# Optimization experiments

Measured on AMD Instinct MI355X. Metric: run time of the kernel, lower is better.

Reference implementation:

```python
import jax, jax.numpy as jnp
import numpy as np

T, B, D = 256, 256, 512
H, DK = 8, 64          # num_heads, d_kv; inner_dim = H*DK = 512
NUM_GROUPS = 16


def setup_inputs() -> dict:
    key = jax.random.key(0)
    ks = jax.random.split(key, 6)
    hidden_states = jax.random.normal(ks[0], (T, B, D), dtype=jnp.float32)
    # sorted group ids over the batch axis (what _infer_group_ids_from_mask recovers)
    group_ids = jnp.sort(jax.random.randint(ks[1], (B,), 0, NUM_GROUPS, dtype=jnp.int32))
    scale = 1.0 / np.sqrt(D)
    Wq = jax.random.normal(ks[2], (D, H * DK), dtype=jnp.float32) * scale
    Wk = jax.random.normal(ks[3], (D, H * DK), dtype=jnp.float32) * scale
    Wv = jax.random.normal(ks[4], (D, H * DK), dtype=jnp.float32) * scale
    Wo = jax.random.normal(ks[5], (H * DK, D), dtype=jnp.float32) * scale
    return {"hidden_states": hidden_states, "group_ids": group_ids,
            "Wq": Wq, "Wk": Wk, "Wv": Wv, "Wo": Wo}


def reference(hidden_states, group_ids, Wq, Wk, Wv, Wo):
    # Group-restricted self-attention along the batch axis, per time step & head.
    # Equivalent to the block-sparse MiniFlash kernel: entries attend only to
    # batch entries with the same group id.
    t, b, d = hidden_states.shape
    q = (hidden_states @ Wq).reshape(t, b, H, DK)
    k = (hidden_states @ Wk).reshape(t, b, H, DK)
    v = (hidden_states @ Wv).reshape(t, b, H, DK)
    sm_scale = 1.0 / np.sqrt(DK)
    # scores: [T, H, B, B] over the batch axis
    scores = jnp.einsum("tihd,tjhd->thij", q, k) * sm_scale
    allowed = group_ids[:, None] == group_ids[None, :]          # [B, B]
    neg = jnp.finfo(scores.dtype).min
    scores = jnp.where(allowed[None, None, :, :], scores, neg)
    attn = jax.nn.softmax(scores, axis=-1)
    out = jnp.einsum("thij,tjhd->tihd", attn, v).reshape(t, b, H * DK)
    return out @ Wo
```

## Files before the change

kernel.cpp:

```cpp
#include <hip/hip_runtime.h>
#include <hip/hip_bf16.h>

typedef __attribute__((ext_vector_type(8))) short short8;
typedef __attribute__((ext_vector_type(4))) short short4v;
typedef __attribute__((ext_vector_type(4))) float f32x4;

#define MFMA16(a, b, c) __builtin_amdgcn_mfma_f32_16x16x32_bf16(a, b, c, 0, 0, 0)

__device__ __forceinline__ unsigned short f2bf(float f) {
    union { __hip_bfloat16 h; unsigned short u; } v;
    v.h = __float2bfloat16(f);
    return v.u;
}

__device__ __forceinline__ short8 pack8(float4 a, float4 b) {
    short8 p;
    p[0] = (short)f2bf(a.x); p[1] = (short)f2bf(a.y);
    p[2] = (short)f2bf(a.z); p[3] = (short)f2bf(a.w);
    p[4] = (short)f2bf(b.x); p[5] = (short)f2bf(b.y);
    p[6] = (short)f2bf(b.z); p[7] = (short)f2bf(b.w);
    return p;
}

__device__ __forceinline__ int swz64(int row, int bytecol) {
    return row * 64 + ((bytecol ^ ((row & 7) << 4)) >> 1);
}
__device__ __forceinline__ int swz256(int row, int bytecol) {
    return row * 256 + ((bytecol ^ ((row & 7) << 4)) >> 1);
}

__global__ __launch_bounds__(256) void wprep(
    const float* __restrict__ Wq, const float* __restrict__ Wk,
    const float* __restrict__ Wv, const float* __restrict__ Wo,
    unsigned short* __restrict__ wt)
{
    __shared__ float tile[64][65];
    const int bid = blockIdx.x;
    const int m = bid >> 6, tb = bid & 63;
    const int kr = (tb >> 3) << 6, nc = (tb & 7) << 6;
    const float* W = (m == 0) ? Wq : (m == 1) ? Wk : (m == 2) ? Wv : Wo;
    const int tid = threadIdx.x;
    for (int i = tid; i < 4096; i += 256)
        tile[i >> 6][i & 63] = W[(size_t)(kr + (i >> 6)) * 512 + nc + (i & 63)];
    __syncthreads();
    unsigned short* dst = wt + (size_t)m * 262144;
    for (int i = tid; i < 4096; i += 256)
        dst[(size_t)(nc + (i >> 6)) * 512 + kr + (i & 63)] = f2bf(tile[i & 63][i >> 6]);
}

__global__ __launch_bounds__(1024, 4) void qkv_attn_mfma(
    const float* __restrict__ hs,
    const int*   __restrict__ gid,
    const float* __restrict__ Wq, const float* __restrict__ Wk,
    const float* __restrict__ Wv,
    const unsigned short* __restrict__ wt,
    float*       __restrict__ out)
{
    __shared__ unsigned short Xs[256 * 64];
    __shared__ unsigned short Wsh[192 * 64];
    __shared__ unsigned short Ksh[256 * 64];
    __shared__ unsigned short Vt[64 * 256];
    __shared__ unsigned short XP[256 * 64];
    __shared__ int sgid[256];
    __shared__ int glo[16], ghi[16];

    const int bid = blockIdx.x;
    const int h   = (bid & 63) >> 3;
    const int t   = ((bid >> 6) << 3) + (bid & 7);

    const int tid  = threadIdx.x;
    const int lane = tid & 63;
    const int w    = tid >> 6;
    const int l15  = lane & 15;
    const int hi4  = lane >> 4;
    const int mg   = w & 3;
    const int ng   = w >> 2;

    if (tid < 16) { glo[tid] = 256; ghi[tid] = -1; }
    __syncthreads();
    if (tid < 256) {
        const int g = gid[tid];
        sgid[tid] = g;
        atomicMin(&glo[g], tid);
        atomicMax(&ghi[g], tid);
    }

    const float* __restrict__ Xbase = hs + (size_t)t * (256 * 512);

    const int xr = tid >> 2, xq = tid & 3;
    const bool doW = tid < 768;
    const int wc = tid >> 2;
    const int wq = tid & 3;
    const int wmat = wc >> 6, wcol = wc & 63;
    const unsigned short* __restrict__ wsrc =
        wt ? wt + ((size_t)wmat * 512 + h * 64 + wcol) * 512 : nullptr;
    const float* __restrict__ wfsrc =
        (wmat == 0) ? Wq : (wmat == 1) ? Wk : Wv;

    f32x4 acc[4][3];
    #pragma unroll
    for (int mt = 0; mt < 4; ++mt)
        #pragma unroll
        for (int nt = 0; nt < 3; ++nt)
            acc[mt][nt] = (f32x4){0.f, 0.f, 0.f, 0.f};

    float4 xf[4];
    short8 w8[2];
    {
        const float* s = Xbase + (size_t)xr * 512 + xq * 16;
        xf[0] = *(const float4*)(s + 0);  xf[1] = *(const float4*)(s + 4);
        xf[2] = *(const float4*)(s + 8);  xf[3] = *(const float4*)(s + 12);
        if (doW) {
            if (wt) {
                w8[0] = *(const short8*)(wsrc + wq * 16);
                w8[1] = *(const short8*)(wsrc + wq * 16 + 8);
            } else {
                #pragma unroll
                for (int b = 0; b < 2; ++b)
                    #pragma unroll
                    for (int j = 0; j < 8; ++j)
                        w8[b][j] = (short)f2bf(
                            wfsrc[(size_t)(wq * 16 + b * 8 + j) * 512 + h * 64 + wcol]);
            }
        }
    }

    for (int kb = 0; kb < 512; kb += 64) {
        *(short8*)&Xs[swz64(xr, xq * 32 + 0)]  = pack8(xf[0], xf[1]);
        *(short8*)&Xs[swz64(xr, xq * 32 + 16)] = pack8(xf[2], xf[3]);
        if (doW) {
            *(short8*)&Wsh[swz64(wc, wq * 32 + 0)]  = w8[0];
            *(short8*)&Wsh[swz64(wc, wq * 32 + 16)] = w8[1];
        }
        __syncthreads();
        if (kb < 448) {
            const int kn = kb + 64;
            const float* s = Xbase + (size_t)xr * 512 + kn + xq * 16;
            xf[0] = *(const float4*)(s + 0);  xf[1] = *(const float4*)(s + 4);
            xf[2] = *(const float4*)(s + 8);  xf[3] = *(const float4*)(s + 12);
            if (doW) {
                if (wt) {
                    w8[0] = *(const short8*)(wsrc + kn + wq * 16);
                    w8[1] = *(const short8*)(wsrc + kn + wq * 16 + 8);
                } else {
                    #pragma unroll
                    for (int b = 0; b < 2; ++b)
                        #pragma unroll
                        for (int j = 0; j < 8; ++j)
                            w8[b][j] = (short)f2bf(
                                wfsrc[(size_t)(kn + wq * 16 + b * 8 + j) * 512 + h * 64 + wcol]);
                }
            }
        }
        #pragma unroll
        for (int ks = 0; ks < 2; ++ks) {
            short8 af[4];
            #pragma unroll
            for (int mt = 0; mt < 4; ++mt)
                af[mt] = *(const short8*)&Xs[swz64(mg * 64 + mt * 16 + l15,
                                                   ks * 64 + hi4 * 16)];
            __builtin_amdgcn_s_setprio(1);
            #pragma unroll
            for (int nt = 0; nt < 3; ++nt) {
                const short8 bf = *(const short8*)&Wsh[swz64(ng * 48 + nt * 16 + l15,
                                                             ks * 64 + hi4 * 16)];
                #pragma unroll
                for (int mt = 0; mt < 4; ++mt)
                    acc[mt][nt] = MFMA16(af[mt], bf, acc[mt][nt]);
            }
            __builtin_amdgcn_s_setprio(0);
        }
        __syncthreads();
    }

    #pragma unroll
    for (int nt = 0; nt < 3; ++nt) {
        const int c0 = (ng * 3 + nt) * 16;
        const int m  = c0 >> 6;
        const int d0 = c0 & 63;
        #pragma unroll
        for (int mt = 0; mt < 4; ++mt) {
            const int rowb = mg * 64 + mt * 16 + hi4 * 4;
            if (m == 0) {
                #pragma unroll
                for (int r = 0; r < 4; ++r)
                    XP[swz64(rowb + r, (d0 + l15) * 2)] = f2bf(acc[mt][nt][r]);
            } else if (m == 1) {
                #pragma unroll
                for (int r = 0; r < 4; ++r)
                    Ksh[swz64(rowb + r, (d0 + l15) * 2)] = f2bf(acc[mt][nt][r]);
            } else {
                short4v vv;
                #pragma unroll
                for (int r = 0; r < 4; ++r) vv[r] = (short)f2bf(acc[mt][nt][r]);
                *(short4v*)&Vt[swz256(d0 + l15, rowb * 2)] = vv;
            }
        }
    }
    __syncthreads();

    const int wrow = w << 4;
    int rg[4];
    #pragma unroll
    for (int r = 0; r < 4; ++r) rg[r] = sgid[wrow + hi4 * 4 + r];
    const int klo = glo[sgid[wrow]];
    const int khi = ghi[sgid[wrow + 15]];

    short8 qf[2];
    #pragma unroll
    for (int ks = 0; ks < 2; ++ks)
        qf[ks] = *(const short8*)&XP[swz64(wrow + l15, ks * 64 + hi4 * 16)];

    f32x4 o[4];
    float mrun[4], lrun[4];
    #pragma unroll
    for (int n = 0; n < 4; ++n) o[n] = (f32x4){0.f, 0.f, 0.f, 0.f};
    #pragma unroll
    for (int r = 0; r < 4; ++r) { mrun[r] = -3.0e38f; lrun[r] = 0.f; }

    for (int kc = klo & ~63; kc <= khi; kc += 64) {
        f32x4 sfr[4];
        __builtin_amdgcn_s_setprio(1);
        #pragma unroll
        for (int n = 0; n < 4; ++n) {
            const int krow = kc + n * 16 + l15;
            const short8 kf0 = *(const short8*)&Ksh[swz64(krow, hi4 * 16)];
            const short8 kf1 = *(const short8*)&Ksh[swz64(krow, 64 + hi4 * 16)];
            f32x4 z = (f32x4){0.f, 0.f, 0.f, 0.f};
            z = MFMA16(qf[0], kf0, z);
            z = MFMA16(qf[1], kf1, z);
            sfr[n] = z;
        }
        __builtin_amdgcn_s_setprio(0);
        int cg[4];
        #pragma unroll
        for (int n = 0; n < 4; ++n) cg[n] = sgid[kc + n * 16 + l15];

        #pragma unroll
        for (int r = 0; r < 4; ++r) {
            const int gr = rg[r];
            float sv[4];
            float smax = -3.0e38f;
            #pragma unroll
            for (int n = 0; n < 4; ++n) {
                float x = sfr[n][r] * 0.125f;
                x = (cg[n] == gr) ? x : -3.0e38f;
                sv[n] = x;
                smax = fmaxf(smax, x);
            }
            smax = fmaxf(smax, __shfl_xor(smax, 1));
            smax = fmaxf(smax, __shfl_xor(smax, 2));
            smax = fmaxf(smax, __shfl_xor(smax, 4));
            smax = fmaxf(smax, __shfl_xor(smax, 8));
            const float newm = fmaxf(mrun[r], smax);
            const float corr = __expf(mrun[r] - newm);
            float ps = 0.f;
            unsigned short pb[4];
            #pragma unroll
            for (int n = 0; n < 4; ++n) {
                const float p = (sv[n] > -1.0e38f) ? __expf(sv[n] - newm) : 0.f;
                ps += p;
                pb[n] = f2bf(p);
            }
            ps += __shfl_xor(ps, 1); ps += __shfl_xor(ps, 2);
            ps += __shfl_xor(ps, 4); ps += __shfl_xor(ps, 8);
            lrun[r] = lrun[r] * corr + ps;
            mrun[r] = newm;
            #pragma unroll
            for (int n = 0; n < 4; ++n) o[n][r] *= corr;
            const int prow = wrow + hi4 * 4 + r;
            #pragma unroll
            for (int n = 0; n < 4; ++n)
                XP[swz64(prow, (n * 16 + l15) * 2)] = pb[n];
        }

        const short8 pa0 = *(const short8*)&XP[swz64(wrow + l15, hi4 * 16)];
        const short8 pa1 = *(const short8*)&XP[swz64(wrow + l15, 64 + hi4 * 16)];
        __builtin_amdgcn_s_setprio(1);
        #pragma unroll
        for (int n = 0; n < 4; ++n) {
            const short8 vb0 = *(const short8*)&Vt[swz256(n * 16 + l15, (kc + hi4 * 8) * 2)];
            const short8 vb1 = *(const short8*)&Vt[swz256(n * 16 + l15, (kc + 32 + hi4 * 8) * 2)];
            o[n] = MFMA16(pa0, vb0, o[n]);
            o[n] = MFMA16(pa1, vb1, o[n]);
        }
        __builtin_amdgcn_s_setprio(0);
    }

    float* __restrict__ op = out + (size_t)t * (256 * 512) + h * 64;
    #pragma unroll
    for (int r = 0; r < 4; ++r) {
        const int row = wrow + hi4 * 4 + r;
        const float inv = 1.0f / lrun[r];
        #pragma unroll
        for (int n = 0; n < 4; ++n)
            op[(size_t)row * 512 + n * 16 + l15] = o[n][r] * inv;
    }
}

__global__ __launch_bounds__(1024, 4) void oproj_mfma(
    const float* __restrict__ Wo,
    const unsigned short* __restrict__ wot,
    float* __restrict__ out)
{
    __shared__ unsigned short As[128 * 40];
    __shared__ unsigned short Bts[512 * 40];

    const int tid  = threadIdx.x;
    const int lane = tid & 63;
    const int w    = tid >> 6;
    const int l15  = lane & 15;
    const int hi4  = lane >> 4;
    const int wr   = w >> 2;
    const int wc   = w & 3;
    const size_t r0 = (size_t)blockIdx.x * 128;

    f32x4 acc[2][8];
    #pragma unroll
    for (int m = 0; m < 2; ++m)
        #pragma unroll
        for (int n = 0; n < 8; ++n)
            acc[m][n] = (f32x4){0.f, 0.f, 0.f, 0.f};

    const bool isA = tid < 512;
    const int bn = tid & 511;
    const int ai = bn >> 2, aq = bn & 3;

    float4 af0, af1;
    short8 b8[4];

    if (isA) {
        const float* s = out + (r0 + ai) * 512 + aq * 8;
        af0 = *(const float4*)s; af1 = *(const float4*)(s + 4);
    } else {
        if (wot) {
            #pragma unroll
            for (int q = 0; q < 4; ++q)
                b8[q] = *(const short8*)(wot + (size_t)bn * 512 + q * 8);
        } else {
            #pragma unroll
            for (int q = 0; q < 4; ++q)
                #pragma unroll
                for (int j = 0; j < 8; ++j)
                    b8[q][j] = (short)f2bf(Wo[(size_t)(q * 8 + j) * 512 + bn]);
        }
    }

    for (int kb = 0; kb < 512; kb += 32) {
        if (isA) *(short8*)&As[ai * 40 + aq * 8] = pack8(af0, af1);
        else {
            #pragma unroll
            for (int q = 0; q < 4; ++q)
                *(short8*)&Bts[bn * 40 + q * 8] = b8[q];
        }
        __syncthreads();
        if (kb < 480) {
            const int kn = kb + 32;
            if (isA) {
                const float* s = out + (r0 + ai) * 512 + kn + aq * 8;
                af0 = *(const float4*)s; af1 = *(const float4*)(s + 4);
            } else {
                if (wot) {
                    #pragma unroll
                    for (int q = 0; q < 4; ++q)
                        b8[q] = *(const short8*)(wot + (size_t)bn * 512 + kn + q * 8);
                } else {
                    #pragma unroll
                    for (int q = 0; q < 4; ++q)
                        #pragma unroll
                        for (int j = 0; j < 8; ++j)
                            b8[q][j] = (short)f2bf(Wo[(size_t)(kn + q * 8 + j) * 512 + bn]);
                }
            }
        }
        short8 afr[2];
        #pragma unroll
        for (int m = 0; m < 2; ++m)
            afr[m] = *(const short8*)&As[(wr * 32 + m * 16 + l15) * 40 + hi4 * 8];
        __builtin_amdgcn_s_setprio(1);
        #pragma unroll
        for (int n = 0; n < 8; ++n) {
            const short8 bfr = *(const short8*)&Bts[(wc * 128 + n * 16 + l15) * 40 + hi4 * 8];
            #pragma unroll
            for (int m = 0; m < 2; ++m)
                acc[m][n] = MFMA16(afr[m], bfr, acc[m][n]);
        }
        __builtin_amdgcn_s_setprio(0);
        __syncthreads();
    }

    #pragma unroll
    for (int m = 0; m < 2; ++m)
        #pragma unroll
        for (int n = 0; n < 8; ++n)
            #pragma unroll
            for (int r = 0; r < 4; ++r)
                out[(r0 + wr * 32 + m * 16 + hi4 * 4 + r) * 512 + wc * 128 + n * 16 + l15] =
                    acc[m][n][r];
}

extern "C" void kernel_launch(void* const* d_in, const int* in_sizes, int n_in,
                              void* d_out, int out_size, void* d_ws, size_t ws_size,
                              hipStream_t stream) {
    const float* hs  = (const float*)d_in[0];
    const int*   gid = (const int*)  d_in[1];
    const float* Wq  = (const float*)d_in[2];
    const float* Wk  = (const float*)d_in[3];
    const float* Wv  = (const float*)d_in[4];
    const float* Wo  = (const float*)d_in[5];
    float* outp = (float*)d_out;

    unsigned short* wt  = nullptr;
    unsigned short* wot = nullptr;
    if (ws_size >= (size_t)4 * 512 * 512 * 2) {
        wt  = (unsigned short*)d_ws;
        wot = wt + (size_t)3 * 512 * 512;
        wprep<<<256, 256, 0, stream>>>(Wq, Wk, Wv, Wo, wt);
    }

    qkv_attn_mfma<<<2048, 1024, 0, stream>>>(hs, gid, Wq, Wk, Wv, wt, outp);
    oproj_mfma<<<512, 1024, 0, stream>>>(Wo, wot, outp);
}
```

Measured before the change: 318.1 us.

## Split fused QKV-attention kernel into a standalone QKV GEMM plus attention kernel

Replaces the fused per-(t,h) QKV projection and attention kernel with two kernels. The first is a large-tile bf16 MFMA GEMM that writes Q, K and V into a workspace in per-(t,h) layout. The second is an attention kernel that reads those tiles and runs the group-restricted online softmax. The aim is to avoid recomputing and reloading X tiles for each head inside the fused kernel and to give the projection better GEMM efficiency. The cost is a large bf16 intermediate written to and read back from global memory, and the split path is only taken when the workspace is big enough.

Measured after the change: 370.7 us. +16.5%, slower.

```diff
diff --git a/kernel.cpp b/kernel.cpp
--- a/kernel.cpp
+++ b/kernel.cpp
@@ -46,6 +46,256 @@
     unsigned short* dst = wt + (size_t)m * 262144;
     for (int i = tid; i < 4096; i += 256)
         dst[(size_t)(nc + (i >> 6)) * 512 + kr + (i & 63)] = f2bf(tile[i & 63][i >> 6]);
+}
+
+__global__ __launch_bounds__(1024, 4) void qkv_gemm(
+    const float* __restrict__ hs,
+    const unsigned short* __restrict__ wt,
+    unsigned short* __restrict__ qkvb)
+{
+    __shared__ unsigned short As[128 * 40];
+    __shared__ unsigned short Bts[512 * 40];
+
+    const int orig = blockIdx.x;
+    const int wg = (orig & 7) * 192 + (orig >> 3);
+    const int mb = wg / 3;
+    const int nb = wg - mb * 3;
+
+    const int tid  = threadIdx.x;
+    const int lane = tid & 63;
+    const int w    = tid >> 6;
+    const int l15  = lane & 15;
+    const int hi4  = lane >> 4;
+    const int wr   = w >> 2, wc = w & 3;
+
+    f32x4 acc[2][8];
+    #pragma unroll
+    for (int m = 0; m < 2; ++m)
+        #pragma unroll
+        for (int n = 0; n < 8; ++n)
+            acc[m][n] = (f32x4){0.f, 0.f, 0.f, 0.f};
+
+    const bool isA = tid < 512;
+    const int bn = tid & 511;
+    const int ai = bn >> 2, aq = bn & 3;
+
+    const float* __restrict__ asrc = hs + ((size_t)mb * 128 + ai) * 512 + aq * 8;
+    const unsigned short* __restrict__ bsrc = wt + ((size_t)nb * 512 + bn) * 512;
+
+    float4 af0, af1;
+    short8 b8[4];
+    if (isA) {
+        af0 = *(const float4*)asrc; af1 = *(const float4*)(asrc + 4);
+    } else {
+        #pragma unroll
+        for (int q = 0; q < 4; ++q) b8[q] = *(const short8*)(bsrc + q * 8);
+    }
+
+    for (int kb = 0; kb < 512; kb += 32) {
+        if (isA) *(short8*)&As[ai * 40 + aq * 8] = pack8(af0, af1);
+        else {
+            #pragma unroll
+            for (int q = 0; q < 4; ++q) *(short8*)&Bts[bn * 40 + q * 8] = b8[q];
+        }
+        __syncthreads();
+        if (kb < 480) {
+            const int kn = kb + 32;
+            if (isA) {
+                af0 = *(const float4*)(asrc + kn);
+                af1 = *(const float4*)(asrc + kn + 4);
+            } else {
+                #pragma unroll
+                for (int q = 0; q < 4; ++q)
+                    b8[q] = *(const short8*)(bsrc + kn + q * 8);
+            }
+        }
+        short8 afr[2];
+        #pragma unroll
+        for (int m = 0; m < 2; ++m)
+            afr[m] = *(const short8*)&As[(wr * 32 + m * 16 + l15) * 40 + hi4 * 8];
+        __builtin_amdgcn_s_setprio(1);
+        #pragma unroll
+        for (int n = 0; n < 8; ++n) {
+            const short8 bfr = *(const short8*)&Bts[(wc * 128 + n * 16 + l15) * 40 + hi4 * 8];
+            #pragma unroll
+            for (int m = 0; m < 2; ++m)
+                acc[m][n] = MFMA16(afr[m], bfr, acc[m][n]);
+        }
+        __builtin_amdgcn_s_setprio(0);
+        __syncthreads();
+    }
+
+    const size_t matoff = (size_t)nb * 33554432;
+    #pragma unroll
+    for (int m = 0; m < 2; ++m) {
+        #pragma unroll
+        for (int n = 0; n < 8; ++n) {
+            const int col = wc * 128 + n * 16 + l15;
+            const int hh = col >> 6, d = col & 63;
+            #pragma unroll
+            for (int r = 0; r < 4; ++r) {
+                const int row = mb * 128 + wr * 32 + m * 16 + hi4 * 4 + r;
+                const int t = row >> 8, i = row & 255;
+                qkvb[matoff + (((size_t)t * 8 + hh) << 14) + (i << 6) + d] =
+                    f2bf(acc[m][n][r]);
+            }
+        }
+    }
+}
+
+__global__ __launch_bounds__(1024, 4) void attn_split(
+    const unsigned short* __restrict__ qkvb,
+    const int* __restrict__ gid,
+    float* __restrict__ out)
+{
+    __shared__ unsigned short Ksh[256 * 64];
+    __shared__ unsigned short Vt[64 * 256];
+    __shared__ unsigned short Ps[256 * 64];
+    __shared__ int sgid[256];
+    __shared__ int glo[16], ghi[16];
+
+    const int th = blockIdx.x;
+    const int t = th >> 3, h = th & 7;
+    const int tid  = threadIdx.x;
+    const int lane = tid & 63;
+    const int w    = tid >> 6;
+    const int l15  = lane & 15;
+    const int hi4  = lane >> 4;
+    const int wrow = w << 4;
+
+    if (tid < 16) { glo[tid] = 256; ghi[tid] = -1; }
+    __syncthreads();
+    if (tid < 256) {
+        const int g = gid[tid];
+        sgid[tid] = g;
+        atomicMin(&glo[g], tid);
+        atomicMax(&ghi[g], tid);
+    }
+
+    const unsigned short* __restrict__ qb = qkvb + ((size_t)th << 14);
+    const unsigned short* __restrict__ kb = qkvb + 33554432ull + ((size_t)th << 14);
+    const unsigned short* __restrict__ vb = qkvb + 67108864ull + ((size_t)th << 14);
+
+    {
+        const int kr = tid >> 2, kq = tid & 3;
+        const short8 k0 = *(const short8*)(kb + kr * 64 + kq * 16);
+        const short8 k1 = *(const short8*)(kb + kr * 64 + kq * 16 + 8);
+        *(short8*)&Ksh[swz64(kr, kq * 32)]      = k0;
+        *(short8*)&Ksh[swz64(kr, kq * 32 + 16)] = k1;
+        const short8 v0 = *(const short8*)(vb + kr * 64 + kq * 16);
+        const short8 v1 = *(const short8*)(vb + kr * 64 + kq * 16 + 8);
+        *(short8*)&Ps[kr * 64 + kq * 16]     = v0;
+        *(short8*)&Ps[kr * 64 + kq * 16 + 8] = v1;
+    }
+    short8 qf[2];
+    #pragma unroll
+    for (int ks = 0; ks < 2; ++ks)
+        qf[ks] = *(const short8*)(qb + (wrow + l15) * 64 + ks * 32 + hi4 * 8);
+    __syncthreads();
+
+    {
+        const int d = tid & 63, jc = tid >> 6;
+        short8 a, b;
+        #pragma unroll
+        for (int jj = 0; jj < 8; ++jj) a[jj] = Ps[(jc * 16 + jj) * 64 + d];
+        #pragma unroll
+        for (int jj = 0; jj < 8; ++jj) b[jj] = Ps[(jc * 16 + 8 + jj) * 64 + d];
+        *(short8*)&Vt[swz256(d, jc * 32)]      = a;
+        *(short8*)&Vt[swz256(d, jc * 32 + 16)] = b;
+    }
+    __syncthreads();
+
+    int rg[4];
+    #pragma unroll
+    for (int r = 0; r < 4; ++r) rg[r] = sgid[wrow + hi4 * 4 + r];
+    const int klo = glo[sgid[wrow]];
+    const int khi = ghi[sgid[wrow + 15]];
+
+    f32x4 o[4];
+    float mrun[4], lrun[4];
+    #pragma unroll
+    for (int n = 0; n < 4; ++n) o[n] = (f32x4){0.f, 0.f, 0.f, 0.f};
+    #pragma unroll
+    for (int r = 0; r < 4; ++r) { mrun[r] = -3.0e38f; lrun[r] = 0.f; }
+
+    for (int kc = klo & ~63; kc <= khi; kc += 64) {
+        f32x4 sfr[4];
+        __builtin_amdgcn_s_setprio(1);
+        #pragma unroll
+        for (int n = 0; n < 4; ++n) {
+            const int krow = kc + n * 16 + l15;
+            const short8 kf0 = *(const short8*)&Ksh[swz64(krow, hi4 * 16)];
+            const short8 kf1 = *(const short8*)&Ksh[swz64(krow, 64 + hi4 * 16)];
+            f32x4 z = (f32x4){0.f, 0.f, 0.f, 0.f};
+            z = MFMA16(qf[0], kf0, z);
+            z = MFMA16(qf[1], kf1, z);
+            sfr[n] = z;
+        }
+        __builtin_amdgcn_s_setprio(0);
+        int cg[4];
+        #pragma unroll
+        for (int n = 0; n < 4; ++n) cg[n] = sgid[kc + n * 16 + l15];
+
+        #pragma unroll
+        for (int r = 0; r < 4; ++r) {
+            const int gr = rg[r];
+            float sv[4];
+            float smax = -3.0e38f;
+            #pragma unroll
+            for (int n = 0; n < 4; ++n) {
+                float x = sfr[n][r] * 0.125f;
+                x = (cg[n] == gr) ? x : -3.0e38f;
+                sv[n] = x;
+                smax = fmaxf(smax, x);
+            }
+            smax = fmaxf(smax, __shfl_xor(smax, 1));
+            smax = fmaxf(smax, __shfl_xor(smax, 2));
+            smax = fmaxf(smax, __shfl_xor(smax, 4));
+            smax = fmaxf(smax, __shfl_xor(smax, 8));
+            const float newm = fmaxf(mrun[r], smax);
+            const float corr = __expf(mrun[r] - newm);
+            float ps = 0.f;
+            unsigned short pb[4];
+            #pragma unroll
+            for (int n = 0; n < 4; ++n) {
+                const float p = (sv[n] > -1.0e38f) ? __expf(sv[n] - newm) : 0.f;
+                ps += p;
+                pb[n] = f2bf(p);
+            }
+            ps += __shfl_xor(ps, 1); ps += __shfl_xor(ps, 2);
+            ps += __shfl_xor(ps, 4); ps += __shfl_xor(ps, 8);
+            lrun[r] = lrun[r] * corr + ps;
+            mrun[r] = newm;
+            #pragma unroll
+            for (int n = 0; n < 4; ++n) o[n][r] *= corr;
+            const int prow = wrow + hi4 * 4 + r;
+            #pragma unroll
+            for (int n = 0; n < 4; ++n)
+                Ps[swz64(prow, (n * 16 + l15) * 2)] = pb[n];
+        }
+
+        const short8 pa0 = *(const short8*)&Ps[swz64(wrow + l15, hi4 * 16)];
+        const short8 pa1 = *(const short8*)&Ps[swz64(wrow + l15, 64 + hi4 * 16)];
+        __builtin_amdgcn_s_setprio(1);
+        #pragma unroll
+        for (int n = 0; n < 4; ++n) {
+            const short8 vb0 = *(const short8*)&Vt[swz256(n * 16 + l15, (kc + hi4 * 8) * 2)];
+            const short8 vb1 = *(const short8*)&Vt[swz256(n * 16 + l15, (kc + 32 + hi4 * 8) * 2)];
+            o[n] = MFMA16(pa0, vb0, o[n]);
+            o[n] = MFMA16(pa1, vb1, o[n]);
+        }
+        __builtin_amdgcn_s_setprio(0);
+    }
+
+    float* __restrict__ op = out + (size_t)t * (256 * 512) + h * 64;
+    #pragma unroll
+    for (int r = 0; r < 4; ++r) {
+        const int row = wrow + hi4 * 4 + r;
+        const float inv = 1.0f / lrun[r];
+        #pragma unroll
+        for (int n = 0; n < 4; ++n)
+            op[(size_t)row * 512 + n * 16 + l15] = o[n][r] * inv;
+    }
 }
 
 __global__ __launch_bounds__(1024, 4) void qkv_attn_mfma(
@@ -410,14 +660,24 @@
     const float* Wo  = (const float*)d_in[5];
     float* outp = (float*)d_out;
 
-    unsigned short* wt  = nullptr;
-    unsigned short* wot = nullptr;
-    if (ws_size >= (size_t)4 * 512 * 512 * 2) {
+    const size_t WT_SHORTS  = 1048576;
+    const size_t QKV_SHORTS = 100663296;
+    unsigned short* wt   = nullptr;
+    unsigned short* wot  = nullptr;
+    unsigned short* qkvb = nullptr;
+    if (ws_size >= WT_SHORTS * 2) {
         wt  = (unsigned short*)d_ws;
-        wot = wt + (size_t)3 * 512 * 512;
+        wot = wt + (size_t)3 * 262144;
         wprep<<<256, 256, 0, stream>>>(Wq, Wk, Wv, Wo, wt);
-    }
-
-    qkv_attn_mfma<<<2048, 1024, 0, stream>>>(hs, gid, Wq, Wk, Wv, wt, outp);
+        if (ws_size >= (WT_SHORTS + QKV_SHORTS) * 2)
+            qkvb = wt + WT_SHORTS;
+    }
+
+    if (qkvb) {
+        qkv_gemm<<<1536, 1024, 0, stream>>>(hs, wt, qkvb);
+        attn_split<<<2048, 1024, 0, stream>>>(qkvb, gid, outp);
+    } else {
+        qkv_attn_mfma<<<2048, 1024, 0, stream>>>(hs, gid, Wq, Wk, Wv, wt, outp);
+    }
     oproj_mfma<<<512, 1024, 0, stream>>>(Wo, wot, outp);
 }
```
